# Kernel tuning notes

Measured on AMD Instinct MI355X. Metric: run time of the kernel, lower is better.

## Reference

```python
import jax, jax.numpy as jnp
import numpy as np

B, N, EG = 4, 16384, 131072
H, DK, DV, DM = 4, 32, 32, 128


def setup_inputs() -> dict:
    key = jax.random.key(0)
    ks = jax.random.split(key, 12)
    s = 0.05
    return {
        "edge_indices": jax.random.randint(ks[0], (B, 2, EG), 0, N, dtype=jnp.int32),
        "edge_features": jax.random.normal(ks[1], (B, EG, DM), jnp.float32),
        "input_Q": jax.random.normal(ks[2], (B, N, DM), jnp.float32),
        "input_K": jax.random.normal(ks[3], (B, N, DM), jnp.float32),
        "input_V": jax.random.normal(ks[4], (B, N, DM), jnp.float32),
        "W_Q": jax.random.normal(ks[5], (DM, H * DK), jnp.float32) * s,
        "W_K": jax.random.normal(ks[6], (DM, H * DK), jnp.float32) * s,
        "W_V": jax.random.normal(ks[7], (DM, H * DV), jnp.float32) * s,
        "W_E": jax.random.normal(ks[8], (DM, H * DV), jnp.float32) * s,
        "W_fc": jax.random.normal(ks[9], (H * DV, DM), jnp.float32) * s,
        "ln_gamma": jnp.ones((DM,), jnp.float32),
        "ln_beta": jnp.zeros((DM,), jnp.float32),
    }


def _layer_norm(x, g, b, eps=1e-5):
    mu = jnp.mean(x, axis=-1, keepdims=True)
    var = jnp.mean(jnp.square(x - mu), axis=-1, keepdims=True)
    return g * (x - mu) * jax.lax.rsqrt(var + eps) + b


def _proj(x, W, d):
    # [B, T, DM] @ [DM, H*d] -> [B, H, T, d]
    bsz, t, _ = x.shape
    return (x @ W).reshape(bsz, t, H, d).transpose(0, 2, 1, 3)


def reference(edge_indices, edge_features, input_Q, input_K, input_V,
              W_Q, W_K, W_V, W_E, W_fc, ln_gamma, ln_beta):
    residual = input_Q
    bsz, n_nodes, _ = input_Q.shape
    Q = _proj(input_Q, W_Q, DK)        # [B,H,N,dk]
    K = _proj(input_K, W_K, DK)
    V = _proj(input_V, W_V, DV)
    E = _proj(edge_features, W_E, DV)  # [B,H,Eg,dv]

    inv_sqrt_dk = 1.0 / np.sqrt(DK).astype(np.float32)

    def one_graph(Qb, Kb, Vb, Eb, idx):
        src, tgt = idx[0], idx[1]                       # [Eg]
        Qe = Qb[:, src]                                  # [H,Eg,dk]
        Ke = Kb[:, tgt]
        Ve = Vb[:, tgt]
        scores = (Qe * Ke) * inv_sqrt_dk * Eb            # [H,Eg,dv]
        attn = jnp.exp(jnp.clip(scores.sum(-1, keepdims=True), -5.0, 5.0))  # [H,Eg,1]
        msg = attn * Ve                                  # [H,Eg,dv]
        num = jnp.zeros((H, n_nodes, DV), Qb.dtype).at[:, src].add(msg)
        den = jnp.zeros((H, n_nodes, 1), Qb.dtype).at[:, src].add(attn)
        return num / (den + 1e-8), attn

    out, attn = jax.vmap(one_graph)(Q, K, V, E, edge_indices)  # [B,H,N,dv], [B,H,Eg,1]

    out = out.transpose(0, 2, 1, 3).reshape(bsz, n_nodes, H * DV)
    out = out @ W_fc
    out = _layer_norm(out + residual, ln_gamma, ln_beta)
    # torch code returns attn from the last batch iteration (leading dim 1)
    return out, attn[-1:]
```

## Files before the change

### kernel.cpp

```cpp
#include <hip/hip_runtime.h>

#define BB 4
#define NN 16384
#define EGc 131072
#define CAP 64
#define INVSQ 0.17677669529663687f

typedef unsigned int uint;
typedef unsigned short ushort;
typedef short short8 __attribute__((ext_vector_type(8)));
typedef float floatx4 __attribute__((ext_vector_type(4)));

__device__ __forceinline__ float bflo(uint u) { return __uint_as_float(u << 16); }
__device__ __forceinline__ float bfhi(uint u) { return __uint_as_float(u & 0xffff0000u); }
__device__ __forceinline__ ushort f2bf(float f) {
    uint u = __float_as_uint(f);
    u += 0x7fffu + ((u >> 16) & 1u);
    return (ushort)(u >> 16);
}

#define SA_STRIDE 136
#define SW_STRIDE 136
#define SY_STRIDE 132
struct __align__(16) SMem {
    union {
        struct {
            ushort sA[64 * SA_STRIDE];
            ushort sW[128 * SW_STRIDE];
        };
        float  sY[64 * SY_STRIDE];
        ushort sOut[64 * 128];
    };
};

__device__ __forceinline__ void stage_x(SMem& sm, const float4* __restrict__ X4,
                                        size_t r0, int t) {
#pragma unroll
    for (int i = 0; i < 8; ++i) {
        int f = t + 256 * i;
        int r = f >> 5, c4 = f & 31;
        float4 x = X4[(r0 + r) * 32 + c4];
        ushort4 h;
        h.x = f2bf(x.x); h.y = f2bf(x.y); h.z = f2bf(x.z); h.w = f2bf(x.w);
        *(ushort4*)&sm.sA[r * SA_STRIDE + c4 * 4] = h;
    }
}

__device__ __forceinline__ void stage_wt(SMem& sm, const uint4* __restrict__ Wt4, int t) {
#pragma unroll
    for (int i = 0; i < 8; ++i) {
        int f = t + 256 * i;
        int c = f >> 4, kc = f & 15;
        uint4 w = Wt4[f];
        *(uint4*)&sm.sW[c * SW_STRIDE + kc * 8] = w;
    }
}

__device__ __forceinline__ void mfma_core(const SMem& sm, int t, floatx4 (&acc)[2][4]) {
    int lane = t & 63, w = t >> 6;
    int wr = (w >> 1) * 32, wc = (w & 1) * 64;
    int m = lane & 15, q = lane >> 4;
#pragma unroll
    for (int ks = 0; ks < 4; ++ks) {
        int k = ks * 32 + q * 8;
        short8 a0 = *(const short8*)&sm.sA[(wr + m) * SA_STRIDE + k];
        short8 a1 = *(const short8*)&sm.sA[(wr + 16 + m) * SA_STRIDE + k];
#pragma unroll
        for (int j = 0; j < 4; ++j) {
            short8 b = *(const short8*)&sm.sW[(wc + j * 16 + m) * SW_STRIDE + k];
            acc[0][j] = __builtin_amdgcn_mfma_f32_16x16x32_bf16(a0, b, acc[0][j], 0, 0, 0);
            acc[1][j] = __builtin_amdgcn_mfma_f32_16x16x32_bf16(a1, b, acc[1][j], 0, 0, 0);
        }
    }
}

__device__ __forceinline__ void acc_zero(floatx4 (&acc)[2][4]) {
    floatx4 z = {0.f, 0.f, 0.f, 0.f};
#pragma unroll
    for (int i = 0; i < 2; ++i)
#pragma unroll
        for (int j = 0; j < 4; ++j) acc[i][j] = z;
}

__device__ __forceinline__ void acc_to_sy(SMem& sm, int t, const floatx4 (&acc)[2][4]) {
    int lane = t & 63, w = t >> 6;
    int wr = (w >> 1) * 32, wc = (w & 1) * 64;
    int m = lane & 15, q = lane >> 4;
#pragma unroll
    for (int i = 0; i < 2; ++i)
#pragma unroll
        for (int j = 0; j < 4; ++j)
#pragma unroll
            for (int r = 0; r < 4; ++r)
                sm.sY[(wr + i * 16 + q * 4 + r) * SY_STRIDE + wc + j * 16 + m] = acc[i][j][r];
}

__global__ __launch_bounds__(256) void transpose_w(const float* __restrict__ W0,
                                                   const float* __restrict__ W1,
                                                   const float* __restrict__ W2,
                                                   const float* __restrict__ W3,
                                                   const float* __restrict__ W4,
                                                   ushort* __restrict__ Wt) {
    __shared__ ushort sT[128 * 136];
    int bi = blockIdx.x;
    const float* W = bi == 0 ? W0 : bi == 1 ? W1 : bi == 2 ? W2 : bi == 3 ? W3 : W4;
    int t = threadIdx.x;
    const float4* Wp = (const float4*)W;
#pragma unroll
    for (int i = 0; i < 16; ++i) {
        int f = t + 256 * i;
        int d = f >> 5, c4 = f & 31;
        float4 w = Wp[f];
        sT[(c4 * 4 + 0) * 136 + d] = f2bf(w.x);
        sT[(c4 * 4 + 1) * 136 + d] = f2bf(w.y);
        sT[(c4 * 4 + 2) * 136 + d] = f2bf(w.z);
        sT[(c4 * 4 + 3) * 136 + d] = f2bf(w.w);
    }
    __syncthreads();
    uint4* out = (uint4*)(Wt + (size_t)bi * 16384);
#pragma unroll
    for (int i = 0; i < 8; ++i) {
        int f = t + 256 * i;
        int c = f >> 4, kc = f & 15;
        out[f] = *(const uint4*)&sT[c * 136 + kc * 8];
    }
}

__global__ __launch_bounds__(256) void proj_mfma(const float* __restrict__ IQ,
                                                 const float* __restrict__ IK,
                                                 const float* __restrict__ IV,
                                                 const ushort* __restrict__ WtAll,
                                                 ushort* __restrict__ Qp,
                                                 ushort* __restrict__ Kp,
                                                 ushort* __restrict__ Vp) {
    __shared__ SMem sm;
    int t = threadIdx.x;
    const float* X; const ushort* Wt; ushort* Y;
    if (blockIdx.y == 0)      { X = IQ; Wt = WtAll;         Y = Qp; }
    else if (blockIdx.y == 1) { X = IK; Wt = WtAll + 16384; Y = Kp; }
    else                      { X = IV; Wt = WtAll + 32768; Y = Vp; }
    size_t r0 = (size_t)blockIdx.x * 64;
    stage_x(sm, (const float4*)X, r0, t);
    stage_wt(sm, (const uint4*)Wt, t);
    __syncthreads();
    floatx4 acc[2][4];
    acc_zero(acc);
    mfma_core(sm, t, acc);
    __syncthreads();
    {
        int lane = t & 63, w = t >> 6;
        int wr = (w >> 1) * 32, wc = (w & 1) * 64;
        int m = lane & 15, q = lane >> 4;
#pragma unroll
        for (int i = 0; i < 2; ++i)
#pragma unroll
            for (int j = 0; j < 4; ++j)
#pragma unroll
                for (int r = 0; r < 4; ++r)
                    sm.sOut[(wr + i * 16 + q * 4 + r) * 128 + wc + j * 16 + m] = f2bf(acc[i][j][r]);
    }
    __syncthreads();
    uint4* Y4 = (uint4*)Y;
#pragma unroll
    for (int i = 0; i < 4; ++i) {
        int f = t + 256 * i;
        Y4[r0 * 16 + f] = *(const uint4*)&sm.sOut[f * 8];
    }
}

__global__ __launch_bounds__(256, 3) void edge_kernel(const int* __restrict__ EI,
                                                      const float* __restrict__ EF,
                                                      const ushort* __restrict__ WtE,
                                                      const ushort* __restrict__ Qp,
                                                      const ushort* __restrict__ Kp,
                                                      float* __restrict__ aArr,
                                                      int* __restrict__ list,
                                                      int* __restrict__ cnt,
                                                      float* __restrict__ attn_out) {
    __shared__ SMem sm;
    int t = threadIdx.x;
    int b = blockIdx.x >> 11;
    int tile = blockIdx.x & 2047;
    int e0 = tile * 64;
    int w = t >> 6, lane = t & 63;

    if (t < 64) {
        int ge = e0 + t;
        int src = EI[(size_t)b * 2 * EGc + ge];
        int tgt = EI[(size_t)b * 2 * EGc + EGc + ge];
        int slot = atomicAdd(&cnt[b * NN + src], 1);
        if (slot < CAP) list[((size_t)(b * NN + src)) * CAP + slot] = (tgt << 17) | ge;
    }

    int e16 = w * 16 + (lane & 15);
    int srcv = EI[(size_t)b * 2 * EGc + e0 + e16];
    int tgtv = EI[(size_t)b * 2 * EGc + EGc + e0 + e16];
    const uint* Qu = (const uint*)Qp;
    const uint* Ku = (const uint*)Kp;
    uint q01[16], k01[16];
#pragma unroll
    for (int ei = 0; ei < 16; ++ei) {
        int s = __shfl(srcv, ei, 16);
        int g = __shfl(tgtv, ei, 16);
        q01[ei] = Qu[((size_t)b * NN + s) * 64 + lane];
        k01[ei] = Ku[((size_t)b * NN + g) * 64 + lane];
    }

    stage_x(sm, (const float4*)EF, (size_t)b * EGc + e0, t);
    stage_wt(sm, (const uint4*)WtE, t);
    __syncthreads();
    floatx4 acc[2][4];
    acc_zero(acc);
    mfma_core(sm, t, acc);
    __syncthreads();
    acc_to_sy(sm, t, acc);
    __syncthreads();

    int h = lane >> 4;
    bool isLast = (b == BB - 1);
#pragma unroll
    for (int ei = 0; ei < 16; ++ei) {
        int e = w * 16 + ei;
        float2 ev = *(const float2*)&sm.sY[e * SY_STRIDE + 2 * lane];
        float p = bflo(q01[ei]) * bflo(k01[ei]) * ev.x + bfhi(q01[ei]) * bfhi(k01[ei]) * ev.y;
        p += __shfl_xor(p, 8, 64);
        p += __shfl_xor(p, 4, 64);
        p += __shfl_xor(p, 2, 64);
        p += __shfl_xor(p, 1, 64);
        float av = __expf(fminf(fmaxf(p * INVSQ, -5.f), 5.f));
        int ge = e0 + e;
        if ((lane & 15) == 0) {
            aArr[((size_t)b * EGc + ge) * 4 + h] = av;
            if (isLast) attn_out[(size_t)h * EGc + ge] = av;
        }
    }
}

__global__ __launch_bounds__(256) void gather_kernel(const ushort* __restrict__ Vp,
                                                     const float* __restrict__ aArr,
                                                     const int* __restrict__ list,
                                                     const int* __restrict__ cnt,
                                                     uint* __restrict__ Xg) {
    int t = threadIdx.x;
    int w = t >> 6, lane = t & 63;
    int wid = blockIdx.x * 4 + w;
    size_t n0 = (size_t)wid * 4;
    int b = (int)(n0 >> 14);
    int h = lane >> 4;
    const uint* Vu = (const uint*)Vp;
    const float* aBase = aArr + (size_t)b * EGc * 4;

    int degv = 0;
    if (lane < 4) degv = cnt[n0 + lane];

    for (int ni = 0; ni < 4; ++ni) {
        size_t grow = n0 + ni;
        int deg = __shfl(degv, ni, 64);
        deg = deg < CAP ? deg : CAP;
        int le = 0, tv = 0;
        if (lane < deg) {
            int pk = list[grow * CAP + lane];
            le = pk & 0x1FFFF;
            tv = pk >> 17;
        }
        float afp0, afp1 = 0.f, afp2 = 0.f, afp3 = 0.f;
        {
            int m0 = __shfl(le, lane & 15, 64);
            afp0 = aBase[(size_t)m0 * 4 + h];
            if (deg > 16) { int m1 = __shfl(le, 16 + (lane & 15), 64); afp1 = aBase[(size_t)m1 * 4 + h]; }
            if (deg > 32) { int m2 = __shfl(le, 32 + (lane & 15), 64); afp2 = aBase[(size_t)m2 * 4 + h]; }
            if (deg > 48) { int m3 = __shfl(le, 48 + (lane & 15), 64); afp3 = aBase[(size_t)m3 * 4 + h]; }
        }
        float n0v = 0.f, n1v = 0.f, dh = 0.f;
#define FCHUNK(K, AFP) \
        if (deg > 16 * K) { \
            int lim = deg - 16 * K; lim = lim > 16 ? 16 : lim; \
            _Pragma("unroll 8") \
            for (int j2 = 0; j2 < lim; ++j2) { \
                int tgt = __shfl(tv, 16 * K + j2, 64); \
                float af = __shfl(AFP, (lane & 48) + j2, 64); \
                uint v01 = Vu[((size_t)b * NN + tgt) * 64 + lane]; \
                n0v += af * bflo(v01); n1v += af * bfhi(v01); dh += af; \
            } \
        }
        FCHUNK(0, afp0)
        FCHUNK(1, afp1)
        FCHUNK(2, afp2)
        FCHUNK(3, afp3)
#undef FCHUNK
        float inv = 1.f / (dh + 1e-8f);
        uint packed = (uint)f2bf(n0v * inv) | ((uint)f2bf(n1v * inv) << 16);
        Xg[grow * 64 + lane] = packed;
    }
}

__global__ __launch_bounds__(256) void fc_ln_kernel(const uint* __restrict__ Xg,
                                                    const ushort* __restrict__ WtFC,
                                                    const float* __restrict__ IQ,
                                                    const float* __restrict__ G,
                                                    const float* __restrict__ Bt,
                                                    float* __restrict__ Out) {
    __shared__ SMem sm;
    int t = threadIdx.x;
    size_t r0 = (size_t)blockIdx.x * 64;
    const uint4* X4 = (const uint4*)(Xg + r0 * 64);
#pragma unroll
    for (int i = 0; i < 4; ++i) {
        int f = t + 256 * i;
        int r = f >> 4, c = f & 15;
        uint4 x = X4[f];
        *(uint4*)&sm.sA[r * SA_STRIDE + c * 8] = x;
    }
    stage_wt(sm, (const uint4*)WtFC, t);
    __syncthreads();
    floatx4 acc[2][4];
    acc_zero(acc);
    mfma_core(sm, t, acc);
    __syncthreads();
    acc_to_sy(sm, t, acc);
    __syncthreads();

    int w = t >> 6, lane = t & 63;
    float g0 = G[lane], g1 = G[lane + 64];
    float be0 = Bt[lane], be1 = Bt[lane + 64];
    for (int ei = 0; ei < 16; ++ei) {
        int e = w * 16 + ei;
        size_t row = r0 + e;
        float y0 = sm.sY[e * SY_STRIDE + lane]      + IQ[row * 128 + lane];
        float y1 = sm.sY[e * SY_STRIDE + lane + 64] + IQ[row * 128 + lane + 64];
        float s = y0 + y1;
        float qq = y0 * y0 + y1 * y1;
#pragma unroll
        for (int off = 32; off >= 1; off >>= 1) {
            s  += __shfl_xor(s, off, 64);
            qq += __shfl_xor(qq, off, 64);
        }
        float mu = s * (1.f / 128.f);
        float var = qq * (1.f / 128.f) - mu * mu;
        float rstd = rsqrtf(var + 1e-5f);
        Out[row * 128 + lane]      = g0 * (y0 - mu) * rstd + be0;
        Out[row * 128 + lane + 64] = g1 * (y1 - mu) * rstd + be1;
    }
}

extern "C" void kernel_launch(void* const* d_in, const int* in_sizes, int n_in,
                              void* d_out, int out_size, void* d_ws, size_t ws_size,
                              hipStream_t stream) {
    const int*   EI  = (const int*)d_in[0];
    const float* EF  = (const float*)d_in[1];
    const float* IQ  = (const float*)d_in[2];
    const float* IK  = (const float*)d_in[3];
    const float* IV  = (const float*)d_in[4];
    const float* WQ  = (const float*)d_in[5];
    const float* WK  = (const float*)d_in[6];
    const float* WV  = (const float*)d_in[7];
    const float* WE  = (const float*)d_in[8];
    const float* WFC = (const float*)d_in[9];
    const float* G   = (const float*)d_in[10];
    const float* Bt  = (const float*)d_in[11];

    char* ws = (char*)d_ws;
    ushort* Qp   = (ushort*)ws;
    ushort* Kp   = (ushort*)(ws + 16777216);
    ushort* Vp   = (ushort*)(ws + 2 * 16777216);
    ushort* Wt   = (ushort*)(ws + 3 * 16777216);
    float*  aArr = (float*) (ws + 3 * 16777216 + 262144);
    int*    list = (int*)   (ws + 3 * 16777216 + 262144 + 8388608);
    int*    cnt  = (int*)   (ws + 4 * 16777216 + 262144 + 8388608);

    float* out0 = (float*)d_out;
    float* attn_out = out0 + (size_t)BB * NN * 128;

    hipMemsetAsync(cnt, 0, (size_t)BB * NN * sizeof(int), stream);

    transpose_w<<<5, 256, 0, stream>>>(WQ, WK, WV, WE, WFC, Wt);

    dim3 pg(1024, 3);
    proj_mfma<<<pg, 256, 0, stream>>>(IQ, IK, IV, Wt, Qp, Kp, Vp);

    edge_kernel<<<BB * (EGc / 64), 256, 0, stream>>>(EI, EF, Wt + 3 * 16384,
                                                     Qp, Kp, aArr, list, cnt, attn_out);

    uint* Xg = (uint*)Qp;
    gather_kernel<<<4096, 256, 0, stream>>>(Vp, aArr, list, cnt, Xg);

    fc_ln_kernel<<<1024, 256, 0, stream>>>(Xg, Wt + 4 * 16384, IQ, G, Bt, out0);
}
```

Before: 574.0 us.

## Scatter attention weights into per-node slot buffer to avoid indirect gather

The edge kernel now writes each edge's attention weight directly into a per-source-node, per-slot buffer (node × CAP × heads) using the slot it got from the atomic counter. This replaces the edge-indexed array the gather kernel had to read indirectly. The gather kernel reads these weights contiguously with a lane permutation and batches its list and weight loads for all four nodes up front. The atomic/list insertion is also moved after the Q/K gathers so those loads can be issued first. The cost is a much larger workspace buffer (64MB), and writes from the edge kernel become scattered.

```diff
diff --git a/kernel.cpp b/kernel.cpp
--- a/kernel.cpp
+++ b/kernel.cpp
@@ -173,24 +173,18 @@
                                                       const ushort* __restrict__ WtE,
                                                       const ushort* __restrict__ Qp,
                                                       const ushort* __restrict__ Kp,
-                                                      float* __restrict__ aArr,
+                                                      float* __restrict__ af_buf,
                                                       int* __restrict__ list,
                                                       int* __restrict__ cnt,
                                                       float* __restrict__ attn_out) {
     __shared__ SMem sm;
+    __shared__ int sSrc[64];
+    __shared__ int sSlot[64];
     int t = threadIdx.x;
     int b = blockIdx.x >> 11;
     int tile = blockIdx.x & 2047;
     int e0 = tile * 64;
     int w = t >> 6, lane = t & 63;
-
-    if (t < 64) {
-        int ge = e0 + t;
-        int src = EI[(size_t)b * 2 * EGc + ge];
-        int tgt = EI[(size_t)b * 2 * EGc + EGc + ge];
-        int slot = atomicAdd(&cnt[b * NN + src], 1);
-        if (slot < CAP) list[((size_t)(b * NN + src)) * CAP + slot] = (tgt << 17) | ge;
-    }
 
     int e16 = w * 16 + (lane & 15);
     int srcv = EI[(size_t)b * 2 * EGc + e0 + e16];
@@ -204,6 +198,16 @@
         int g = __shfl(tgtv, ei, 16);
         q01[ei] = Qu[((size_t)b * NN + s) * 64 + lane];
         k01[ei] = Ku[((size_t)b * NN + g) * 64 + lane];
+    }
+
+    if (t < 64) {
+        int ge = e0 + t;
+        int src = EI[(size_t)b * 2 * EGc + ge];
+        int tgt = EI[(size_t)b * 2 * EGc + EGc + ge];
+        int slot = atomicAdd(&cnt[b * NN + src], 1);
+        sSrc[t] = src;
+        sSlot[t] = slot;
+        if (slot < CAP) list[((size_t)(b * NN + src)) * CAP + slot] = (tgt << 17) | ge;
     }
 
     stage_x(sm, (const float4*)EF, (size_t)b * EGc + e0, t);
@@ -228,16 +232,17 @@
         p += __shfl_xor(p, 2, 64);
         p += __shfl_xor(p, 1, 64);
         float av = __expf(fminf(fmaxf(p * INVSQ, -5.f), 5.f));
-        int ge = e0 + e;
         if ((lane & 15) == 0) {
-            aArr[((size_t)b * EGc + ge) * 4 + h] = av;
-            if (isLast) attn_out[(size_t)h * EGc + ge] = av;
+            int slot = sSlot[e];
+            if (slot < CAP)
+                af_buf[((size_t)(b * NN + sSrc[e])) * (CAP * 4) + slot * 4 + h] = av;
+            if (isLast) attn_out[(size_t)h * EGc + (e0 + e)] = av;
         }
     }
 }
 
 __global__ __launch_bounds__(256) void gather_kernel(const ushort* __restrict__ Vp,
-                                                     const float* __restrict__ aArr,
+                                                     const float* __restrict__ af_buf,
                                                      const int* __restrict__ list,
                                                      const int* __restrict__ cnt,
                                                      uint* __restrict__ Xg) {
@@ -246,51 +251,57 @@
     int wid = blockIdx.x * 4 + w;
     size_t n0 = (size_t)wid * 4;
     int b = (int)(n0 >> 14);
-    int h = lane >> 4;
     const uint* Vu = (const uint*)Vp;
-    const float* aBase = aArr + (size_t)b * EGc * 4;
+    int perm = (lane & 15) * 4 + (lane >> 4);
 
     int degv = 0;
     if (lane < 4) degv = cnt[n0 + lane];
-
+    int deg[4];
+#pragma unroll
     for (int ni = 0; ni < 4; ++ni) {
-        size_t grow = n0 + ni;
-        int deg = __shfl(degv, ni, 64);
-        deg = deg < CAP ? deg : CAP;
-        int le = 0, tv = 0;
-        if (lane < deg) {
-            int pk = list[grow * CAP + lane];
-            le = pk & 0x1FFFF;
-            tv = pk >> 17;
-        }
-        float afp0, afp1 = 0.f, afp2 = 0.f, afp3 = 0.f;
-        {
-            int m0 = __shfl(le, lane & 15, 64);
-            afp0 = aBase[(size_t)m0 * 4 + h];
-            if (deg > 16) { int m1 = __shfl(le, 16 + (lane & 15), 64); afp1 = aBase[(size_t)m1 * 4 + h]; }
-            if (deg > 32) { int m2 = __shfl(le, 32 + (lane & 15), 64); afp2 = aBase[(size_t)m2 * 4 + h]; }
-            if (deg > 48) { int m3 = __shfl(le, 48 + (lane & 15), 64); afp3 = aBase[(size_t)m3 * 4 + h]; }
-        }
+        int d = __shfl(degv, ni, 64);
+        deg[ni] = d < CAP ? d : CAP;
+    }
+
+    int tv[4];
+#pragma unroll
+    for (int ni = 0; ni < 4; ++ni) {
+        tv[ni] = 0;
+        if (lane < deg[ni]) tv[ni] = list[(n0 + ni) * CAP + lane] >> 17;
+    }
+    float afp[4][4];
+#pragma unroll
+    for (int ni = 0; ni < 4; ++ni) {
+        const float* ab = af_buf + (n0 + ni) * (CAP * 4);
+        afp[ni][0] = ab[perm];
+        afp[ni][1] = deg[ni] > 16 ? ab[64 + perm]  : 0.f;
+        afp[ni][2] = deg[ni] > 32 ? ab[128 + perm] : 0.f;
+        afp[ni][3] = deg[ni] > 48 ? ab[192 + perm] : 0.f;
+    }
+
+#pragma unroll
+    for (int ni = 0; ni < 4; ++ni) {
+        int d = deg[ni];
         float n0v = 0.f, n1v = 0.f, dh = 0.f;
-#define FCHUNK(K, AFP) \
-        if (deg > 16 * K) { \
-            int lim = deg - 16 * K; lim = lim > 16 ? 16 : lim; \
+#define FCHUNK(K) \
+        if (d > 16 * K) { \
+            int lim = d - 16 * K; lim = lim > 16 ? 16 : lim; \
             _Pragma("unroll 8") \
             for (int j2 = 0; j2 < lim; ++j2) { \
-                int tgt = __shfl(tv, 16 * K + j2, 64); \
-                float af = __shfl(AFP, (lane & 48) + j2, 64); \
+                int tgt = __shfl(tv[ni], 16 * K + j2, 64); \
+                float af = __shfl(afp[ni][K], (lane & 48) + j2, 64); \
                 uint v01 = Vu[((size_t)b * NN + tgt) * 64 + lane]; \
                 n0v += af * bflo(v01); n1v += af * bfhi(v01); dh += af; \
             } \
         }
-        FCHUNK(0, afp0)
-        FCHUNK(1, afp1)
-        FCHUNK(2, afp2)
-        FCHUNK(3, afp3)
+        FCHUNK(0)
+        FCHUNK(1)
+        FCHUNK(2)
+        FCHUNK(3)
 #undef FCHUNK
         float inv = 1.f / (dh + 1e-8f);
         uint packed = (uint)f2bf(n0v * inv) | ((uint)f2bf(n1v * inv) << 16);
-        Xg[grow * 64 + lane] = packed;
+        Xg[(n0 + ni) * 64 + lane] = packed;
     }
 }
 
@@ -360,13 +371,13 @@
     const float* Bt  = (const float*)d_in[11];
 
     char* ws = (char*)d_ws;
-    ushort* Qp   = (ushort*)ws;
-    ushort* Kp   = (ushort*)(ws + 16777216);
-    ushort* Vp   = (ushort*)(ws + 2 * 16777216);
-    ushort* Wt   = (ushort*)(ws + 3 * 16777216);
-    float*  aArr = (float*) (ws + 3 * 16777216 + 262144);
-    int*    list = (int*)   (ws + 3 * 16777216 + 262144 + 8388608);
-    int*    cnt  = (int*)   (ws + 4 * 16777216 + 262144 + 8388608);
+    ushort* Qp     = (ushort*)ws;
+    ushort* Kp     = (ushort*)(ws + 16777216);
+    ushort* Vp     = (ushort*)(ws + 2 * 16777216);
+    ushort* Wt     = (ushort*)(ws + 3 * 16777216);
+    float*  af_buf = (float*) (ws + 3 * 16777216 + 262144);
+    int*    list   = (int*)   (ws + 3 * 16777216 + 262144 + 67108864);
+    int*    cnt    = (int*)   (ws + 3 * 16777216 + 262144 + 67108864 + 16777216);
 
     float* out0 = (float*)d_out;
     float* attn_out = out0 + (size_t)BB * NN * 128;
@@ -379,10 +390,10 @@
     proj_mfma<<<pg, 256, 0, stream>>>(IQ, IK, IV, Wt, Qp, Kp, Vp);
 
     edge_kernel<<<BB * (EGc / 64), 256, 0, stream>>>(EI, EF, Wt + 3 * 16384,
-                                                     Qp, Kp, aArr, list, cnt, attn_out);
+                                                     Qp, Kp, af_buf, list, cnt, attn_out);
 
     uint* Xg = (uint*)Qp;
-    gather_kernel<<<4096, 256, 0, stream>>>(Vp, aArr, list, cnt, Xg);
+    gather_kernel<<<4096, 256, 0, stream>>>(Vp, af_buf, list, cnt, Xg);
 
     fc_ln_kernel<<<1024, 256, 0, stream>>>(Xg, Wt + 4 * 16384, IQ, G, Bt, out0);
 }
```

Result: slower. 587.7 us (+2.4%).
